# Kernel optimization log

Measured on AMD Instinct MI355X. Metric: run time of the kernel, lower is better.

## Reference

```python
import jax, jax.numpy as jnp
import numpy as np

H = 6  # num_heads
D = 384  # embedding_dim


def _rot(seg, coord):
    # seg: [BN, H, T, L], coord: [BN, T]; rotate interleaved even/odd pairs
    L = seg.shape[-1]
    pairs = max(L // 2, 1)
    inv_freq = 1.0 / (10000.0 ** (jnp.arange(pairs, dtype=seg.dtype) / pairs))
    ang = coord[..., None] * inv_freq          # [BN, T, pairs]
    cos = jnp.cos(ang)[:, None]                # [BN, 1, T, pairs]
    sin = jnp.sin(ang)[:, None]
    even, odd = seg[..., 0::2], seg[..., 1::2]
    re = even * cos - odd * sin
    ro = even * sin + odd * cos
    return jnp.stack((re, ro), axis=-1).reshape(seg.shape)


def _apply_rope3(t, pos, chunk):
    # t: [BN, H, T, Hd], pos: [BN, T, 3]; three axis chunks, tail untouched
    parts, s = [], 0
    for i in range(3):
        parts.append(_rot(t[..., s:s + chunk], pos[..., i]))
        s += chunk
    parts.append(t[..., s:])
    return jnp.concatenate(parts, axis=-1)


def setup_inputs() -> dict:
    key = jax.random.key(0)
    ks = jax.random.split(key, 10)
    B, N, T = 8, 64, 128
    scale = 1.0 / np.sqrt(D)
    return {
        "padded_batches": jax.random.normal(ks[0], (B, N, T, D), jnp.float32),
        "sum_token": jax.random.normal(ks[1], (B, N, 1, D), jnp.float32),
        "positions_3d": jax.random.uniform(ks[2], (B, N, T, 3), jnp.float32),
        "Wq": jax.random.normal(ks[3], (D, D), jnp.float32) * scale,
        "bq": jax.random.normal(ks[4], (D,), jnp.float32) * scale,
        "Wk": jax.random.normal(ks[5], (D, D), jnp.float32) * scale,
        "bk": jax.random.normal(ks[6], (D,), jnp.float32) * scale,
        "Wv": jax.random.normal(ks[7], (D, D), jnp.float32) * scale,
        "bv": jax.random.normal(ks[8], (D,), jnp.float32) * scale,
        "masks": jax.random.randint(ks[9], (B, N, T), 0, 2, jnp.int32),
    }


def reference(padded_batches, sum_token, positions_3d, Wq, bq, Wk, bk, Wv, bv, masks):
    B, N, T, Dm = padded_batches.shape
    Hd = Dm // H
    chunk = Hd // 6 * 2

    # masked mean-pool summary token (summary_mode='avg')
    w = masks[..., None].astype(padded_batches.dtype)          # [B,N,T,1]
    denom = jnp.clip(w.sum(axis=-2, keepdims=True), 1e-6, None)
    summary = (padded_batches * w).sum(axis=-2, keepdims=True) / denom  # [B,N,1,D]

    q = (padded_batches @ Wq + bq).reshape(B * N, T, H, Hd).transpose(0, 2, 1, 3)  # [BN,H,T,Hd]
    k = (summary @ Wk + bk).reshape(B * N, 1, H, Hd).transpose(0, 2, 1, 3)         # [BN,H,1,Hd]
    v = (summary @ Wv + bv).reshape(B * N, 1, H, Hd).transpose(0, 2, 1, 3)

    # 3-axis RoPE on q (token positions) and k (pooled positions)
    pos_summary = (positions_3d * w).sum(axis=-2, keepdims=True) / denom  # [B,N,1,3]
    pos_q = positions_3d.reshape(B * N, T, 3)
    pos_k = pos_summary.reshape(B * N, 1, 3)
    q = _apply_rope3(q, pos_q, chunk)
    k = _apply_rope3(k, pos_k, chunk)

    # SDPA with T queries vs 1 key
    scores = jnp.einsum('bhtd,bhkd->bhtk', q, k) / np.float32(np.sqrt(Hd))  # [BN,H,T,1]
    mask_add = jnp.where(masks.reshape(B * N, 1, T, 1) == 0,
                         jnp.finfo(jnp.float32).min, 0.0)
    attn_w = jax.nn.softmax(scores + mask_add, axis=-1)
    attn = jnp.einsum('bhtk,bhkd->bhtd', attn_w, v)  # [BN,H,T,Hd]

    out = attn.transpose(0, 2, 1, 3).reshape(B, N, T, Dm) + padded_batches
    return out
```

## Files before the change

### kernel.cpp

```cpp
#include <hip/hip_runtime.h>
#include <hip/hip_bf16.h>


#define DM 384
#define TT 128

__global__ __launch_bounds__(DM) void gmha_collapsed_kernel(
    const float* __restrict__ padded,
    const float* __restrict__ Wv,
    const float* __restrict__ bv,
    const int*   __restrict__ masks,
    float*       __restrict__ out)
{
    const int bn = blockIdx.x;
    const int d  = threadIdx.x;

    __shared__ float w_sh[TT];
    __shared__ float summ_sh[DM];

    const float* __restrict__ p = padded + (size_t)bn * TT * DM;
    float*       __restrict__ o = out    + (size_t)bn * TT * DM;

    if (d < TT) w_sh[d] = (float)masks[bn * TT + d];
    __syncthreads();

    float wsum = 0.f;
    #pragma unroll
    for (int t = 0; t < TT; ++t) wsum += w_sh[t];
    const float denom = fmaxf(wsum, 1e-6f);

    float s = 0.f;
    #pragma unroll 8
    for (int t = 0; t < TT; ++t) {
        s += p[(size_t)t * DM + d] * w_sh[t];
    }
    const float summ = s / denom;
    summ_sh[d] = summ;
    __syncthreads();

    float acc = bv[d];
    #pragma unroll 8
    for (int e = 0; e < DM; ++e) {
        acc += summ_sh[e] * Wv[(size_t)e * DM + d];
    }

    #pragma unroll 8
    for (int t = 0; t < TT; ++t) {
        o[(size_t)t * DM + d] = p[(size_t)t * DM + d] + acc;
    }
}

extern "C" void kernel_launch(void* const* d_in, const int* in_sizes, int n_in,
                              void* d_out, int out_size, void* d_ws, size_t ws_size,
                              hipStream_t stream) {
    const float* padded = (const float*)d_in[0];
    const float* Wv     = (const float*)d_in[7];
    const float* bv     = (const float*)d_in[8];
    const int*   masks  = (const int*)d_in[9];
    float* out = (float*)d_out;

    const int BN = 8 * 64;
    gmha_collapsed_kernel<<<BN, DM, 0, stream>>>(padded, Wv, bv, masks, out);
}
```

Before: 243.2 us.

## Vectorize pooling, Wv GEMV and residual add with float4 and split reductions

Threads now handle float4 column groups, with the 384 threads split into 4 row groups. The masked pooling, the summary·Wv matvec and the residual add all use 128-bit loads and stores. Partial sums from the row groups are combined in shared memory, which adds extra syncs. The aim is fewer memory instructions and more bytes in flight per instruction on a bandwidth-bound kernel.

```diff
diff --git a/kernel.cpp b/kernel.cpp
--- a/kernel.cpp
+++ b/kernel.cpp
@@ -4,8 +4,9 @@
 
 #define DM 384
 #define TT 128
+#define C4 96
 
-__global__ __launch_bounds__(DM) void gmha_collapsed_kernel(
+__global__ __launch_bounds__(384) void gmha_v2_kernel(
     const float* __restrict__ padded,
     const float* __restrict__ Wv,
     const float* __restrict__ bv,
@@ -13,40 +14,80 @@
     float*       __restrict__ out)
 {
     const int bn = blockIdx.x;
-    const int d  = threadIdx.x;
+    const int t  = threadIdx.x;
+    const int c  = t % C4;
+    const int r  = t / C4;
 
-    __shared__ float w_sh[TT];
-    __shared__ float summ_sh[DM];
+    __shared__ float  w_sh[TT];
+    __shared__ float4 part_sh[4][C4];
+    __shared__ float  summ_sh[DM];
+    __shared__ float4 v_sh[C4];
 
-    const float* __restrict__ p = padded + (size_t)bn * TT * DM;
-    float*       __restrict__ o = out    + (size_t)bn * TT * DM;
+    const float4* __restrict__ p4 = (const float4*)(padded + (size_t)bn * TT * DM);
+    float4*       __restrict__ o4 = (float4*)(out    + (size_t)bn * TT * DM);
 
-    if (d < TT) w_sh[d] = (float)masks[bn * TT + d];
+    if (t < TT) w_sh[t] = (float)masks[bn * TT + t];
     __syncthreads();
 
     float wsum = 0.f;
     #pragma unroll
-    for (int t = 0; t < TT; ++t) wsum += w_sh[t];
-    const float denom = fmaxf(wsum, 1e-6f);
+    for (int i = 0; i < TT; ++i) wsum += w_sh[i];
+    const float inv_denom = 1.0f / fmaxf(wsum, 1e-6f);
 
-    float s = 0.f;
+    float4 acc = make_float4(0.f, 0.f, 0.f, 0.f);
     #pragma unroll 8
-    for (int t = 0; t < TT; ++t) {
-        s += p[(size_t)t * DM + d] * w_sh[t];
+    for (int tt = r; tt < TT; tt += 4) {
+        const float  w = w_sh[tt];
+        const float4 x = p4[tt * C4 + c];
+        acc.x += x.x * w; acc.y += x.y * w; acc.z += x.z * w; acc.w += x.w * w;
     }
-    const float summ = s / denom;
-    summ_sh[d] = summ;
+    part_sh[r][c] = acc;
     __syncthreads();
 
-    float acc = bv[d];
+    if (t < C4) {
+        const float4 a0 = part_sh[0][t], a1 = part_sh[1][t];
+        const float4 a2 = part_sh[2][t], a3 = part_sh[3][t];
+        float4 s;
+        s.x = (a0.x + a1.x + a2.x + a3.x) * inv_denom;
+        s.y = (a0.y + a1.y + a2.y + a3.y) * inv_denom;
+        s.z = (a0.z + a1.z + a2.z + a3.z) * inv_denom;
+        s.w = (a0.w + a1.w + a2.w + a3.w) * inv_denom;
+        ((float4*)summ_sh)[t] = s;
+    }
+    __syncthreads();
+
+    float4 vacc = make_float4(0.f, 0.f, 0.f, 0.f);
+    const int e0 = r * 96;
     #pragma unroll 8
-    for (int e = 0; e < DM; ++e) {
-        acc += summ_sh[e] * Wv[(size_t)e * DM + d];
+    for (int i = 0; i < 96; ++i) {
+        const int   e  = e0 + i;
+        const float se = summ_sh[e];
+        const float4 wv = *(const float4*)(Wv + (size_t)e * DM + 4 * c);
+        vacc.x += se * wv.x; vacc.y += se * wv.y;
+        vacc.z += se * wv.z; vacc.w += se * wv.w;
     }
+    part_sh[r][c] = vacc;
+    __syncthreads();
 
+    if (t < C4) {
+        const float4 a0 = part_sh[0][t], a1 = part_sh[1][t];
+        const float4 a2 = part_sh[2][t], a3 = part_sh[3][t];
+        const float4 b  = ((const float4*)bv)[t];
+        float4 v;
+        v.x = a0.x + a1.x + a2.x + a3.x + b.x;
+        v.y = a0.y + a1.y + a2.y + a3.y + b.y;
+        v.z = a0.z + a1.z + a2.z + a3.z + b.z;
+        v.w = a0.w + a1.w + a2.w + a3.w + b.w;
+        v_sh[t] = v;
+    }
+    __syncthreads();
+
+    const float4 v = v_sh[c];
     #pragma unroll 8
-    for (int t = 0; t < TT; ++t) {
-        o[(size_t)t * DM + d] = p[(size_t)t * DM + d] + acc;
+    for (int tt = r; tt < TT; tt += 4) {
+        float4 x = p4[tt * C4 + c];
+        x.x += v.x; x.y += v.y; x.z += v.z; x.w += v.w;
+        o4[tt * C4 + c] = x;
     }
 }
 
@@ -60,5 +101,5 @@
     float* out = (float*)d_out;
 
     const int BN = 8 * 64;
-    gmha_collapsed_kernel<<<BN, DM, 0, stream>>>(padded, Wv, bv, masks, out);
+    gmha_v2_kernel<<<BN, 384, 0, stream>>>(padded, Wv, bv, masks, out);
 }
```

Result: faster. 228.6 us (-6.0%).
